# Kernel tuning notes

Hardware: AMD Instinct MI355X
Metric: run time of the kernel (lower is better)

Reference implementation:

```python
import jax, jax.numpy as jnp
import numpy as np

B, L, H = 8, 4096, 1024


def setup_inputs() -> dict:
    key = jax.random.key(0)
    k1, k2 = jax.random.split(key)
    sequence_output = jax.random.normal(k1, (B, L, H), dtype=jnp.float32)
    # each wordpiece position maps to the token it belongs to (monotone non-decreasing)
    wordpiece_to_token = jnp.sort(
        jax.random.randint(k2, (B, L), 0, L, dtype=jnp.int32), axis=-1
    )
    return {"sequence_output": sequence_output, "wordpiece_to_token": wordpiece_to_token}


def reference(sequence_output, wordpiece_to_token):
    # output[b, t, :] = sum over wordpieces w with wordpiece_to_token[b, w] == t
    b_, l_, h_ = sequence_output.shape
    # offset segment ids per batch element so one flat segment_sum handles all
    seg = (wordpiece_to_token.astype(jnp.int32) + jnp.arange(b_, dtype=jnp.int32)[:, None] * l_)
    out = jax.ops.segment_sum(
        sequence_output.reshape(b_ * l_, h_), seg.reshape(-1), num_segments=b_ * l_
    )
    return out.reshape(b_, l_, h_)
```

## Files before the change

### kernel.cpp

```cpp
#include <hip/hip_runtime.h>
#include <hip/hip_bf16.h>


#define B_DIM 8
#define L_DIM 4096
#define H_DIM 1024

__global__ __launch_bounds__(256) void token_seg_sum_kernel(
    const float* __restrict__ seq,
    const int* __restrict__ tok,
    float* __restrict__ out)
{
    const int bt = blockIdx.x;
    const int b  = bt >> 12;
    const int t  = bt & (L_DIM - 1);

    const int* __restrict__ idx = tok + (size_t)b * L_DIM;

    int lo = 0, hi = L_DIM;
    while (lo < hi) {
        int mid = (lo + hi) >> 1;
        if (idx[mid] < t) lo = mid + 1; else hi = mid;
    }
    const int start = lo;
    hi = L_DIM;
    while (lo < hi) {
        int mid = (lo + hi) >> 1;
        if (idx[mid] <= t) lo = mid + 1; else hi = mid;
    }
    const int end = lo;

    const int tid = threadIdx.x;
    const float4* __restrict__ base =
        (const float4*)(seq + (size_t)b * L_DIM * H_DIM);

    float4 acc = make_float4(0.f, 0.f, 0.f, 0.f);
    for (int w = start; w < end; ++w) {
        float4 v = base[(size_t)w * (H_DIM / 4) + tid];
        acc.x += v.x; acc.y += v.y; acc.z += v.z; acc.w += v.w;
    }

    ((float4*)out)[(size_t)bt * (H_DIM / 4) + tid] = acc;
}

extern "C" void kernel_launch(void* const* d_in, const int* in_sizes, int n_in,
                              void* d_out, int out_size, void* d_ws, size_t ws_size,
                              hipStream_t stream) {
    const float* seq = (const float*)d_in[0];
    const int*   tok = (const int*)d_in[1];
    float*       out = (float*)d_out;

    dim3 grid(B_DIM * L_DIM);
    dim3 block(256);
    token_seg_sum_kernel<<<grid, block, 0, stream>>>(seq, tok, out);
}
```

Baseline: 251.8 us.

## Precompute segment start offsets in a prepass instead of per-block binary search

Adds a small kernel that scatters, for each token, the index of its first wordpiece into a workspace array of size L+1 per batch row. The main reduction kernel then reads two offsets instead of running two serial binary searches over global memory per block. This removes a chain of dependent global loads from every block's prologue. In exchange it adds a second launch and relies on the workspace buffer.

```diff
diff --git a/kernel.cpp b/kernel.cpp
--- a/kernel.cpp
+++ b/kernel.cpp
@@ -5,37 +5,46 @@
 #define B_DIM 8
 #define L_DIM 4096
 #define H_DIM 1024
+#define LP1   (L_DIM + 1)
+
+__global__ __launch_bounds__(256) void build_starts_kernel(
+    const int* __restrict__ tok,
+    int* __restrict__ start)
+{
+    const int gid = blockIdx.x * 256 + threadIdx.x;
+    const int b = gid >> 12;
+    const int w = gid & (L_DIM - 1);
+
+    const int* __restrict__ row = tok + (size_t)b * L_DIM;
+    const int cur  = row[w];
+    const int prev = (w > 0) ? row[w - 1] : -1;
+
+    int* __restrict__ srow = start + (size_t)b * LP1;
+    for (int t = prev + 1; t <= cur; ++t) srow[t] = w;
+    if (w == L_DIM - 1) {
+        for (int t = cur + 1; t <= L_DIM; ++t) srow[t] = L_DIM;
+    }
+}
 
 __global__ __launch_bounds__(256) void token_seg_sum_kernel(
     const float* __restrict__ seq,
-    const int* __restrict__ tok,
+    const int* __restrict__ start,
     float* __restrict__ out)
 {
     const int bt = blockIdx.x;
     const int b  = bt >> 12;
     const int t  = bt & (L_DIM - 1);
 
-    const int* __restrict__ idx = tok + (size_t)b * L_DIM;
-
-    int lo = 0, hi = L_DIM;
-    while (lo < hi) {
-        int mid = (lo + hi) >> 1;
-        if (idx[mid] < t) lo = mid + 1; else hi = mid;
-    }
-    const int start = lo;
-    hi = L_DIM;
-    while (lo < hi) {
-        int mid = (lo + hi) >> 1;
-        if (idx[mid] <= t) lo = mid + 1; else hi = mid;
-    }
-    const int end = lo;
+    const int* __restrict__ srow = start + (size_t)b * LP1;
+    const int s = srow[t];
+    const int e = srow[t + 1];
 
     const int tid = threadIdx.x;
     const float4* __restrict__ base =
         (const float4*)(seq + (size_t)b * L_DIM * H_DIM);
 
     float4 acc = make_float4(0.f, 0.f, 0.f, 0.f);
-    for (int w = start; w < end; ++w) {
+    for (int w = s; w < e; ++w) {
         float4 v = base[(size_t)w * (H_DIM / 4) + tid];
         acc.x += v.x; acc.y += v.y; acc.z += v.z; acc.w += v.w;
     }
@@ -49,8 +58,8 @@
     const float* seq = (const float*)d_in[0];
     const int*   tok = (const int*)d_in[1];
     float*       out = (float*)d_out;
+    int*         start = (int*)d_ws;
 
-    dim3 grid(B_DIM * L_DIM);
-    dim3 block(256);
-    token_seg_sum_kernel<<<grid, block, 0, stream>>>(seq, tok, out);
+    build_starts_kernel<<<dim3(B_DIM * L_DIM / 256), dim3(256), 0, stream>>>(tok, start);
+    token_seg_sum_kernel<<<dim3(B_DIM * L_DIM), dim3(256), 0, stream>>>(seq, start, out);
 }
```

Result: faster. 232.7 us (-7.6%).
